# Kernel optimization log

Hardware: AMD Instinct MI355X
Metric: run time of the kernel (lower is better)

## Reference

```python
import jax, jax.numpy as jnp
import numpy as np

M0, M1 = 16, 8            # scalar / vector multiplicities of node_irreps (16x0e + 8x1o)
N_NODES = 10000
N_EDGES = 160000
H_EDGE = 64
W_NUMEL = M0*M0 + M1*M0 + M0*M1 + M1*M1  # 576 per-edge TP weights
EPS = 1e-5


def setup_inputs() -> dict:
    key = jax.random.key(0)
    ks = jax.random.split(key, 8)
    return {
        "node_features": jax.random.normal(ks[0], (N_NODES, M0 + 3*M1), jnp.float32),
        "edge_features": jax.random.normal(ks[1], (N_EDGES, H_EDGE), jnp.float32),
        "edge_sh": jax.random.normal(ks[2], (N_EDGES, 4), jnp.float32),
        "edge_index": jax.random.randint(ks[3], (2, N_EDGES), 0, N_NODES),
        "fc_w1": jax.random.normal(ks[4], (H_EDGE, H_EDGE), jnp.float32) / np.sqrt(H_EDGE),
        "fc_b1": jnp.zeros((H_EDGE,), jnp.float32),
        "fc_w2": jax.random.normal(ks[5], (H_EDGE, W_NUMEL), jnp.float32) / np.sqrt(H_EDGE),
        "fc_b2": jnp.zeros((W_NUMEL,), jnp.float32),
        "bn_w_s": jnp.ones((M0,), jnp.float32),
        "bn_b_s": jnp.zeros((M0,), jnp.float32),
        "bn_w_v": jnp.ones((M1,), jnp.float32),
    }


def reference(node_features, edge_features, edge_sh, edge_index,
              fc_w1, fc_b1, fc_w2, fc_b2, bn_w_s, bn_b_s, bn_w_v):
    N = node_features.shape[0]
    E = edge_features.shape[0]
    edge_dst, edge_src = edge_index[0], edge_index[1]

    # per-edge TP weights from a small MLP on edge features
    w = jax.nn.relu(edge_features @ fc_w1 + fc_b1) @ fc_w2 + fc_b2  # [E, 576]

    # gather node features on destination side
    x = node_features[edge_dst]                      # [E, 40]
    x0 = x[:, :M0]                                   # [E, 16] scalars (0e)
    x1 = x[:, M0:].reshape(E, M1, 3)                 # [E, 8, 3] vectors (1o)
    sh0 = edge_sh[:, 0]                              # [E] l=0
    sh1 = edge_sh[:, 1:4]                            # [E, 3] l=1

    # split per-edge weights by tensor-product path
    o1 = M0*M0; o2 = o1 + M1*M0; o3 = o2 + M0*M1
    w00 = w[:, :o1].reshape(E, M0, M0)               # 0e x 0e -> 0e
    w11 = w[:, o1:o2].reshape(E, M1, M0)             # 1o x 1o -> 0e
    w01 = w[:, o2:o3].reshape(E, M0, M1)             # 0e x 1o -> 1o
    w10 = w[:, o3:].reshape(E, M1, M1)               # 1o x 0e -> 1o

    inv3 = 1.0 / np.sqrt(3.0)                        # w3j(1,1,0) coefficient
    alpha = 1.0 / np.sqrt(M0 + M1)                   # path fan-in normalization

    out0 = (jnp.einsum('eu,euv->ev', x0 * sh0[:, None], w00)
            + inv3 * jnp.einsum('eui,ei,euv->ev', x1, sh1, w11)) * alpha   # [E, 16]
    out1 = (jnp.einsum('eu,ei,euv->evi', x0, sh1, w01)
            + jnp.einsum('e,eui,euv->evi', sh0, x1, w10)) * alpha          # [E, 8, 3]

    tp = jnp.concatenate([out0, out1.reshape(E, 3*M1)], axis=-1)           # [E, 40]

    # scatter_mean over source nodes
    seg = jax.ops.segment_sum(tp, edge_src, num_segments=N)                # [N, 40]
    cnt = jax.ops.segment_sum(jnp.ones((E, 1), tp.dtype), edge_src, num_segments=N)
    out = seg / jnp.maximum(cnt, 1.0)

    # residual (pad is zero-width since tp output irreps == node irreps)
    out = out + node_features

    # e3nn-style BatchNorm (training mode, component normalization)
    s = out[:, :M0]
    v = out[:, M0:].reshape(N, M1, 3)
    mu = s.mean(axis=0)
    s = s - mu
    var = (s * s).mean(axis=0)
    s = s * (jax.lax.rsqrt(var + EPS) * bn_w_s) + bn_b_s
    vnorm = (v * v).mean(axis=-1).mean(axis=0)       # [M1]
    v = v * (jax.lax.rsqrt(vnorm + EPS) * bn_w_v)[None, :, None]
    out = jnp.concatenate([s, v.reshape(N, 3*M1)], axis=-1)

    return out, edge_features
```

## Files before the change

kernel.cpp:

```cpp
#include <hip/hip_runtime.h>

typedef __attribute__((ext_vector_type(8))) short short8;
typedef __attribute__((ext_vector_type(4))) float f32x4;
typedef __attribute__((ext_vector_type(4))) ushort u16x4;

constexpr int NN = 10000;
constexpr int NE = 160000;
constexpr int NT = NE / 16;
constexpr int TPSTR = 64;
constexpr int GBLK = 625;
constexpr float EPSV = 1e-5f;
constexpr float INV3 = 0.57735026918962576f;
constexpr float ALPHA = 0.20412414523193152f;

__device__ __forceinline__ ushort f2bf(float x) {
  unsigned u = __float_as_uint(x);
  u += 0x7fffu + ((u >> 16) & 1u);
  return (ushort)(u >> 16);
}
__device__ __forceinline__ float bf2f(ushort u) {
  return __uint_as_float(((unsigned)u) << 16);
}
__device__ __forceinline__ f32x4 mfma16(short8 a, short8 b, f32x4 c) {
  return __builtin_amdgcn_mfma_f32_16x16x32_bf16(a, b, c, 0, 0, 0);
}
__device__ __forceinline__ void st4u(ushort* p, f32x4 v) {
  u16x4 o;
#pragma unroll
  for (int j = 0; j < 4; ++j) o[j] = f2bf(v[j]);
  *(u16x4*)p = o;
}

constexpr int PREP_DEGB = (NN + 63) / 64;
__global__ __launch_bounds__(64) void prep_w2(const float* __restrict__ w2,
                                              short8* __restrict__ w2bf,
                                              int* __restrict__ deg,
                                              const float* __restrict__ b2,
                                              float* __restrict__ flag) {
  int b = blockIdx.x;
  int lane = threadIdx.x;
  if (b < 72) {
    int jt = b >> 1, kc = b & 1;
    int g = lane >> 4, c = lane & 15;
    short8 v;
#pragma unroll
    for (int j = 0; j < 8; ++j)
      v[j] = (short)f2bf(w2[(kc * 32 + 8 * g + j) * 576 + jt * 16 + c]);
    w2bf[(jt * 2 + kc) * 64 + lane] = v;
  } else if (b < 72 + PREP_DEGB) {
    int idx = (b - 72) * 64 + lane;
    if (idx < NN) deg[idx] = 0;
  } else {
    float m = 0.f;
    for (int i = lane; i < 576; i += 64) m = fmaxf(m, fabsf(b2[i]));
#pragma unroll
    for (int off = 1; off < 64; off <<= 1) m = fmaxf(m, __shfl_xor(m, off));
    if (lane == 0) *flag = m;
  }
}

constexpr int CSTR = 68;
constexpr unsigned SM_W2 = 4608 * 16;
constexpr unsigned SM_B2 = 576 * 4;
constexpr unsigned SM_W1 = 512 * 16;
constexpr unsigned SM_B1 = 64 * 4;
constexpr unsigned SM_HL = 8 * 16 * 72 * 2;
constexpr unsigned SM_SCR = 8 * 16 * CSTR * 4;
constexpr unsigned SM_TOTAL = SM_W2 + SM_B2 + SM_W1 + SM_B1 + SM_HL + SM_SCR;

__global__ __launch_bounds__(512) void conv_kernel(
    const float* __restrict__ ef, const float* __restrict__ w1,
    const float* __restrict__ b1, const short8* __restrict__ w2bf,
    const float* __restrict__ b2, const float* __restrict__ nf,
    const float* __restrict__ sh, const int* __restrict__ ei,
    const int* __restrict__ perm, float* __restrict__ efout, int do_copy,
    ushort* __restrict__ tp, const float* __restrict__ flagp)
{
  extern __shared__ char smem[];
  short8* w2lds = (short8*)smem;
  float*  b2lds = (float*)(smem + SM_W2);
  short8* w1f   = (short8*)(smem + SM_W2 + SM_B2);
  float*  b1lds = (float*)(smem + SM_W2 + SM_B2 + SM_W1);
  ushort* hlall = (ushort*)(smem + SM_W2 + SM_B2 + SM_W1 + SM_B1);
  float*  scrall = (float*)(smem + SM_W2 + SM_B2 + SM_W1 + SM_B1 + SM_HL);

  const int tid = threadIdx.x;
  for (int i = tid; i < 4608; i += 512) w2lds[i] = w2bf[i];
  for (int i = tid; i < 576; i += 512) b2lds[i] = b2[i];
  {
    int tile = tid >> 6, l = tid & 63;
    int nt = tile >> 1, kc = tile & 1;
    int gg = l >> 4, cc = l & 15;
    short8 v;
#pragma unroll
    for (int j = 0; j < 8; ++j)
      v[j] = (short)f2bf(w1[(kc * 32 + 8 * gg + j) * 64 + nt * 16 + cc]);
    w1f[tid] = v;
  }
  if (tid < 64) b1lds[tid] = b1[tid];
  const bool nob2 = (*flagp == 0.f);
  __syncthreads();

  const int lane = tid & 63, wid = tid >> 6;
  const int g = lane >> 4, c = lane & 15;
  const int gh = g >> 1;
  const int e = lane >> 2, part = lane & 3;
  float* scr = scrall + wid * (16 * CSTR);
  ushort* hl = hlall + wid * (16 * 72);

  for (int t = blockIdx.x * 8 + wid; t < NT; t += gridDim.x * 8) {
    const int ege = t * 16 + e;
    const float* __restrict__ src = nf + (size_t)ei[ege] * 40;
    const f32x4 sv = *(const f32x4*)(sh + (size_t)ege * 4);
    const f32x4 v0 = *(const f32x4*)(src + part * 4);
    const f32x4 v1 = *(const f32x4*)(src + 16 + part * 4);
    f32x4 v2 = {};
    if (part < 2) v2 = *(const f32x4*)(src + 32 + part * 4);

    const long ebase = (long)t * 16;
    short8 af[2];
    const float* rowp = ef + (ebase + c) * 64;
#pragma unroll
    for (int kc = 0; kc < 2; ++kc) {
      const f32x4* p = (const f32x4*)(rowp + kc * 32 + 8 * g);
      f32x4 lo = p[0], hi = p[1];
      if (do_copy) {
        f32x4* q = (f32x4*)(efout + (ebase + c) * 64 + kc * 32 + 8 * g);
        q[0] = lo; q[1] = hi;
      }
      short8 v;
#pragma unroll
      for (int j = 0; j < 4; ++j) { v[j] = (short)f2bf(lo[j]); v[4 + j] = (short)f2bf(hi[j]); }
      af[kc] = v;
    }
    f32x4 hacc[4] = {};
#pragma unroll
    for (int nt = 0; nt < 4; ++nt)
#pragma unroll
      for (int kc = 0; kc < 2; ++kc)
        hacc[nt] = mfma16(af[kc], w1f[(nt * 2 + kc) * 64 + lane], hacc[nt]);

#pragma unroll
    for (int nt = 0; nt < 4; ++nt) {
      float bv = b1lds[nt * 16 + c];
#pragma unroll
      for (int q = 0; q < 4; ++q) {
        float h = fmaxf(hacc[nt][q] + bv, 0.f);
        hl[(4 * g + q) * 72 + nt * 16 + c] = f2bf(h);
      }
    }
    const short8 h0 = *(const short8*)&hl[c * 72 + 8 * g];
    const short8 h1 = *(const short8*)&hl[c * 72 + 32 + 8 * g];

    {
      float* ce = scr + e * CSTR;
      f32x4 a0;
#pragma unroll
      for (int q = 0; q < 4; ++q) a0[q] = sv[0] * v0[q];
      *(f32x4*)(ce + 4 * part) = a0;
      *(f32x4*)(ce + 24 + 4 * part) = v0;
      *(f32x4*)(ce + 40 + 4 * part) = v1;
      if (part < 2) *(f32x4*)(ce + 56 + 4 * part) = v2;
#pragma unroll
      for (int uu = 0; uu < 2; ++uu) {
        int u = 2 * part + uu;
        ce[16 + u] = INV3 * (ce[40 + 3 * u] * sv[1] + ce[41 + 3 * u] * sv[2] +
                             ce[42 + 3 * u] * sv[3]);
      }
    }
    const float* __restrict__ cc = scr + c * CSTR;

    f32x4 out0acc = {0.f, 0.f, 0.f, 0.f};
    f32x4 c0acc = {0.f, 0.f, 0.f, 0.f};
    f32x4 c1acc[3] = {};

    if (nob2) {
#pragma unroll
      for (int j4 = 0; j4 < 4; ++j4) {
        const f32x4 a4 = *(const f32x4*)&cc[j4 * 4];
#pragma unroll
        for (int jj = 0; jj < 4; ++jj) {
          const int jt = j4 * 4 + jj;
          f32x4 z = {0.f, 0.f, 0.f, 0.f};
          f32x4 d0 = mfma16(w2lds[(jt * 2 + 0) * 64 + lane], h0, z);
          f32x4 d1 = mfma16(w2lds[(jt * 2 + 1) * 64 + lane], h1, z);
          float a = a4[jj];
#pragma unroll
          for (int q = 0; q < 4; ++q) {
            out0acc[q] = fmaf(a, d0[q], out0acc[q]);
            out0acc[q] = fmaf(a, d1[q], out0acc[q]);
          }
        }
      }
#pragma unroll
      for (int j4 = 0; j4 < 2; ++j4) {
        const f32x4 a4 = *(const f32x4*)&cc[16 + j4 * 4];
#pragma unroll
        for (int jj = 0; jj < 4; ++jj) {
          const int jt = 16 + j4 * 4 + jj;
          f32x4 z = {0.f, 0.f, 0.f, 0.f};
          f32x4 d0 = mfma16(w2lds[(jt * 2 + 0) * 64 + lane], h0, z);
          f32x4 d1 = mfma16(w2lds[(jt * 2 + 1) * 64 + lane], h1, z);
          float a = a4[jj];
#pragma unroll
          for (int q = 0; q < 4; ++q) {
            out0acc[q] = fmaf(a, d0[q], out0acc[q]);
            out0acc[q] = fmaf(a, d1[q], out0acc[q]);
          }
        }
      }
#pragma unroll
      for (int jt = 24; jt < 32; ++jt) {
        f32x4 z = {0.f, 0.f, 0.f, 0.f};
        f32x4 d0 = mfma16(w2lds[(jt * 2 + 0) * 64 + lane], h0, z);
        f32x4 d1 = mfma16(w2lds[(jt * 2 + 1) * 64 + lane], h1, z);
        float a = cc[24 + 2 * (jt - 24) + gh];
#pragma unroll
        for (int q = 0; q < 4; ++q) {
          c0acc[q] = fmaf(a, d0[q], c0acc[q]);
          c0acc[q] = fmaf(a, d1[q], c0acc[q]);
        }
      }
#pragma unroll
      for (int jt = 32; jt < 36; ++jt) {
        f32x4 z = {0.f, 0.f, 0.f, 0.f};
        f32x4 d0 = mfma16(w2lds[(jt * 2 + 0) * 64 + lane], h0, z);
        f32x4 d1 = mfma16(w2lds[(jt * 2 + 1) * 64 + lane], h1, z);
        const int ub = 40 + 3 * (2 * (jt - 32) + gh);
#pragma unroll
        for (int i = 0; i < 3; ++i) {
          float a = cc[ub + i];
#pragma unroll
          for (int q = 0; q < 4; ++q) {
            c1acc[i][q] = fmaf(a, d0[q], c1acc[i][q]);
            c1acc[i][q] = fmaf(a, d1[q], c1acc[i][q]);
          }
        }
      }
    } else {
#pragma unroll
      for (int jt = 0; jt < 16; ++jt) {
        f32x4 d = *(const f32x4*)&b2lds[jt * 16 + 4 * g];
        d = mfma16(w2lds[(jt * 2 + 0) * 64 + lane], h0, d);
        d = mfma16(w2lds[(jt * 2 + 1) * 64 + lane], h1, d);
        float a = cc[jt];
#pragma unroll
        for (int q = 0; q < 4; ++q) out0acc[q] = fmaf(a, d[q], out0acc[q]);
      }
#pragma unroll
      for (int jt = 16; jt < 24; ++jt) {
        f32x4 d = *(const f32x4*)&b2lds[jt * 16 + 4 * g];
        d = mfma16(w2lds[(jt * 2 + 0) * 64 + lane], h0, d);
        d = mfma16(w2lds[(jt * 2 + 1) * 64 + lane], h1, d);
        float a = cc[16 + (jt - 16)];
#pragma unroll
        for (int q = 0; q < 4; ++q) out0acc[q] = fmaf(a, d[q], out0acc[q]);
      }
#pragma unroll
      for (int jt = 24; jt < 32; ++jt) {
        f32x4 d = *(const f32x4*)&b2lds[jt * 16 + 4 * g];
        d = mfma16(w2lds[(jt * 2 + 0) * 64 + lane], h0, d);
        d = mfma16(w2lds[(jt * 2 + 1) * 64 + lane], h1, d);
        float a = cc[24 + 2 * (jt - 24) + gh];
#pragma unroll
        for (int q = 0; q < 4; ++q) c0acc[q] = fmaf(a, d[q], c0acc[q]);
      }
#pragma unroll
      for (int jt = 32; jt < 36; ++jt) {
        f32x4 d = *(const f32x4*)&b2lds[jt * 16 + 4 * g];
        d = mfma16(w2lds[(jt * 2 + 0) * 64 + lane], h0, d);
        d = mfma16(w2lds[(jt * 2 + 1) * 64 + lane], h1, d);
        const int ub = 40 + 3 * (2 * (jt - 32) + gh);
#pragma unroll
        for (int i = 0; i < 3; ++i) {
          float a = cc[ub + i];
#pragma unroll
          for (int q = 0; q < 4; ++q) c1acc[i][q] = fmaf(a, d[q], c1acc[i][q]);
        }
      }
    }

#pragma unroll
    for (int q = 0; q < 4; ++q) c0acc[q] += __shfl_xor(c0acc[q], 32);
#pragma unroll
    for (int i = 0; i < 3; ++i)
#pragma unroll
      for (int q = 0; q < 4; ++q) c1acc[i][q] += __shfl_xor(c1acc[i][q], 32);

    const int eg = t * 16 + c;
    const f32x4 shv = *(const f32x4*)(sh + (size_t)eg * 4);
    ushort* tpr = tp + (size_t)perm[eg] * TPSTR;
    f32x4 o0;
#pragma unroll
    for (int q = 0; q < 4; ++q) o0[q] = ALPHA * out0acc[q];
    st4u(tpr + 4 * g, o0);
    if (g < 2) {
      float wv[12];
#pragma unroll
      for (int q = 0; q < 4; ++q)
#pragma unroll
        for (int i = 0; i < 3; ++i)
          wv[q * 3 + i] = ALPHA * (shv[1 + i] * c0acc[q] + shv[0] * c1acc[i][q]);
#pragma unroll
      for (int p = 0; p < 3; ++p) {
        f32x4 v = {wv[4 * p], wv[4 * p + 1], wv[4 * p + 2], wv[4 * p + 3]};
        st4u(tpr + 16 + 12 * g + 4 * p, v);
      }
    }
  }
}

__global__ __launch_bounds__(256) void hist_kernel(const int* __restrict__ ei,
                                                   int* __restrict__ deg) {
  for (int e = blockIdx.x * 256 + threadIdx.x; e < NE; e += gridDim.x * 256)
    atomicAdd(&deg[ei[NE + e]], 1);
}

__global__ __launch_bounds__(1024) void scan_kernel(const int* __restrict__ deg,
                                                    int* __restrict__ rowoff,
                                                    int* __restrict__ wcur) {
  __shared__ int wsum[16];
  const int t = threadIdx.x;
  const int lane = t & 63, wid = t >> 6;
  const int base = t * 10;
  int d[10];
  int sum = 0;
#pragma unroll
  for (int j = 0; j < 10; ++j) {
    int n = base + j;
    d[j] = (n < NN) ? deg[n] : 0;
    sum += d[j];
  }
  int val = sum;
#pragma unroll
  for (int off = 1; off < 64; off <<= 1) {
    int v = __shfl_up(val, off);
    if (lane >= off) val += v;
  }
  if (lane == 63) wsum[wid] = val;
  __syncthreads();
  if (t < 16) {
    int v = wsum[t];
#pragma unroll
    for (int off = 1; off < 16; off <<= 1) {
      int u = __shfl_up(v, off);
      if (t >= off) v += u;
    }
    wsum[t] = v;
  }
  __syncthreads();
  const int waveoff = (wid > 0) ? wsum[wid - 1] : 0;
  int run = waveoff + (val - sum);
#pragma unroll
  for (int j = 0; j < 10; ++j) {
    int n = base + j;
    if (n < NN) { rowoff[n] = run; wcur[n] = run; }
    run += d[j];
  }
  if (t == 1023) rowoff[NN] = run;
}

__global__ __launch_bounds__(256) void fill_kernel(const int* __restrict__ ei,
                                                   int* __restrict__ wcur,
                                                   int* __restrict__ perm) {
  for (int e = blockIdx.x * 256 + threadIdx.x; e < NE; e += gridDim.x * 256) {
    int pos = atomicAdd(&wcur[ei[NE + e]], 1);
    perm[e] = pos;
  }
}

__global__ __launch_bounds__(256) void gather_kernel(
    const ushort* __restrict__ tp, const int* __restrict__ rowoff,
    const float* __restrict__ nf, float* __restrict__ pre,
    float* __restrict__ pstats)
{
  __shared__ float ls[40];
  const int tid = threadIdx.x;
  if (tid < 40) ls[tid] = 0.f;
  __syncthreads();
  const int wid = tid >> 6, lane = tid & 63;
  float sacc = 0.f, qacc = 0.f;
  if (lane < 40) {
#pragma unroll 1
    for (int i = 0; i < 4; ++i) {
      const int n = blockIdx.x * 16 + wid * 4 + i;
      const int r0 = rowoff[n], r1 = rowoff[n + 1];
      float s0 = 0.f, s1 = 0.f, s2 = 0.f, s3 = 0.f,
            s4 = 0.f, s5 = 0.f, s6 = 0.f, s7 = 0.f;
      int k = r0;
      for (; k + 8 <= r1; k += 8) {
        s0 += bf2f(tp[(size_t)(k + 0) * TPSTR + lane]);
        s1 += bf2f(tp[(size_t)(k + 1) * TPSTR + lane]);
        s2 += bf2f(tp[(size_t)(k + 2) * TPSTR + lane]);
        s3 += bf2f(tp[(size_t)(k + 3) * TPSTR + lane]);
        s4 += bf2f(tp[(size_t)(k + 4) * TPSTR + lane]);
        s5 += bf2f(tp[(size_t)(k + 5) * TPSTR + lane]);
        s6 += bf2f(tp[(size_t)(k + 6) * TPSTR + lane]);
        s7 += bf2f(tp[(size_t)(k + 7) * TPSTR + lane]);
      }
      for (; k < r1; ++k) s0 += bf2f(tp[(size_t)k * TPSTR + lane]);
      float s = ((s0 + s1) + (s2 + s3)) + ((s4 + s5) + (s6 + s7));
      float val = s / fmaxf((float)(r1 - r0), 1.f) + nf[(size_t)n * 40 + lane];
      pre[(size_t)n * 40 + lane] = val;
      if (lane < 16) { sacc += val; qacc += val * val; }
      else qacc += val * val;
    }
    if (lane < 16) {
      atomicAdd(&ls[lane], sacc);
      atomicAdd(&ls[16 + lane], qacc);
    } else {
      atomicAdd(&ls[32 + (lane - 16) / 3], qacc);
    }
  }
  __syncthreads();
  if (tid < 40) pstats[(size_t)blockIdx.x * 40 + tid] = ls[tid];
}

__global__ __launch_bounds__(256) void stats_reduce(
    const float* __restrict__ pstats, float* __restrict__ stats)
{
  const int c = blockIdx.x;
  float s = 0.f;
  for (int i = threadIdx.x; i < GBLK; i += 256) s += pstats[(size_t)i * 40 + c];
#pragma unroll
  for (int off = 1; off < 64; off <<= 1) s += __shfl_xor(s, off);
  __shared__ float red[4];
  if ((threadIdx.x & 63) == 0) red[threadIdx.x >> 6] = s;
  __syncthreads();
  if (threadIdx.x == 0) stats[c] = (red[0] + red[1]) + (red[2] + red[3]);
}

__global__ __launch_bounds__(256) void node_pass2(
    const float* __restrict__ pre, const float* __restrict__ stats,
    const float* __restrict__ bnws, const float* __restrict__ bnbs,
    const float* __restrict__ bnwv, float* __restrict__ out)
{
  int idx = blockIdx.x * blockDim.x + threadIdx.x;
  if (idx >= NN * 40) return;
  int n = idx / 40;
  int c = idx - n * 40;
  float val = pre[idx];
  constexpr float invN = 1.0f / NN;
  if (c < 16) {
    float mu = stats[c] * invN;
    float var = stats[16 + c] * invN - mu * mu;
    out[idx] = (val - mu) * (rsqrtf(var + EPSV) * bnws[c]) + bnbs[c];
  } else {
    int u = (c - 16) / 3;
    float vn = stats[32 + u] * (invN / 3.0f);
    out[idx] = val * (rsqrtf(vn + EPSV) * bnwv[u]);
  }
}

__global__ __launch_bounds__(256) void copy_ef(const f32x4* __restrict__ src,
                                               f32x4* __restrict__ dst) {
  const int n4 = NE * 64 / 4;
  for (int i = blockIdx.x * blockDim.x + threadIdx.x; i < n4;
       i += gridDim.x * blockDim.x)
    dst[i] = src[i];
}

extern "C" void kernel_launch(void* const* d_in, const int* in_sizes, int n_in,
                              void* d_out, int out_size, void* d_ws, size_t ws_size,
                              hipStream_t stream) {
  (void)in_sizes; (void)n_in; (void)out_size;
  const float* nf   = (const float*)d_in[0];
  const float* ef   = (const float*)d_in[1];
  const float* sh   = (const float*)d_in[2];
  const int*   ei   = (const int*)d_in[3];
  const float* w1   = (const float*)d_in[4];
  const float* b1   = (const float*)d_in[5];
  const float* w2   = (const float*)d_in[6];
  const float* b2   = (const float*)d_in[7];
  const float* bnws = (const float*)d_in[8];
  const float* bnbs = (const float*)d_in[9];
  const float* bnwv = (const float*)d_in[10];

  float* out = (float*)d_out;
  float* efout = out + (size_t)NN * 40;

  char* w = (char*)d_ws;
  int* deg     = (int*)w;
  float* stats = (float*)(w + (size_t)NN * 4);
  float* flag  = stats + 44;
  int* rowoff  = (int*)(w + (size_t)NN * 4 + 192);
  int* wcur    = rowoff + NN + 1;
  int* perm    = wcur + NN;
  float* pre   = (float*)(perm + NE);
  float* pstats = pre + (size_t)NN * 40;
  size_t base  = ((size_t)((char*)(pstats + (size_t)GBLK * 40) - w) + 255) & ~(size_t)255;
  short8* w2bf = (short8*)(w + base);
  size_t tpoff = (base + SM_W2 + 255) & ~(size_t)255;

  const size_t TPB = (size_t)NE * TPSTR * 2;
  const size_t needA = tpoff + TPB;

  hipFuncSetAttribute((const void*)conv_kernel,
                      hipFuncAttributeMaxDynamicSharedMemorySize, SM_TOTAL);

  prep_w2<<<72 + PREP_DEGB + 1, 64, 0, stream>>>(w2, w2bf, deg, b2, flag);

  const int pblocks = (NN * 40 + 255) / 256;

  hist_kernel<<<625, 256, 0, stream>>>(ei, deg);
  scan_kernel<<<1, 1024, 0, stream>>>(deg, rowoff, wcur);
  fill_kernel<<<625, 256, 0, stream>>>(ei, wcur, perm);

  if (ws_size >= needA) {
    ushort* tp = (ushort*)(w + tpoff);
    conv_kernel<<<256, 512, SM_TOTAL, stream>>>(
        ef, w1, b1, w2bf, b2, nf, sh, ei, perm, efout, 1, tp, flag);
    gather_kernel<<<GBLK, 256, 0, stream>>>(tp, rowoff, nf, pre, pstats);
    stats_reduce<<<40, 256, 0, stream>>>(pstats, stats);
    node_pass2<<<pblocks, 256, 0, stream>>>(pre, stats, bnws, bnbs, bnwv, out);
  } else {
    ushort* tp = (ushort*)efout;
    conv_kernel<<<256, 512, SM_TOTAL, stream>>>(
        ef, w1, b1, w2bf, b2, nf, sh, ei, perm, efout, 0, tp, flag);
    gather_kernel<<<GBLK, 256, 0, stream>>>(tp, rowoff, nf, pre, pstats);
    stats_reduce<<<40, 256, 0, stream>>>(pstats, stats);
    node_pass2<<<pblocks, 256, 0, stream>>>(pre, stats, bnws, bnbs, bnwv, out);
    copy_ef<<<2048, 256, 0, stream>>>((const f32x4*)ef, (f32x4*)efout);
  }
}
```

Baseline: 94.87 us.

## Switch conv kernel to 32x32 MFMA tiles with atomic work-stealing over edge tiles

```diff
diff --git a/kernel.cpp b/kernel.cpp
--- a/kernel.cpp
+++ b/kernel.cpp
@@ -2,11 +2,12 @@
 
 typedef __attribute__((ext_vector_type(8))) short short8;
 typedef __attribute__((ext_vector_type(4))) float f32x4;
+typedef __attribute__((ext_vector_type(16))) float f32x16;
 typedef __attribute__((ext_vector_type(4))) ushort u16x4;
 
 constexpr int NN = 10000;
 constexpr int NE = 160000;
-constexpr int NT = NE / 16;
+constexpr int NT32 = NE / 32;
 constexpr int TPSTR = 64;
 constexpr int GBLK = 625;
 constexpr float EPSV = 1e-5f;
@@ -21,8 +22,8 @@
 __device__ __forceinline__ float bf2f(ushort u) {
   return __uint_as_float(((unsigned)u) << 16);
 }
-__device__ __forceinline__ f32x4 mfma16(short8 a, short8 b, f32x4 c) {
-  return __builtin_amdgcn_mfma_f32_16x16x32_bf16(a, b, c, 0, 0, 0);
+__device__ __forceinline__ f32x16 mfma32(short8 a, short8 b, f32x16 c) {
+  return __builtin_amdgcn_mfma_f32_32x32x16_bf16(a, b, c, 0, 0, 0);
 }
 __device__ __forceinline__ void st4u(ushort* p, f32x4 v) {
   u16x4 o;
@@ -36,17 +37,18 @@
                                               short8* __restrict__ w2bf,
                                               int* __restrict__ deg,
                                               const float* __restrict__ b2,
-                                              float* __restrict__ flag) {
+                                              float* __restrict__ flag,
+                                              int* __restrict__ wsctr) {
   int b = blockIdx.x;
   int lane = threadIdx.x;
   if (b < 72) {
-    int jt = b >> 1, kc = b & 1;
-    int g = lane >> 4, c = lane & 15;
+    int jt = b >> 2, kt = b & 3;
+    int hi = lane >> 5, cc = lane & 31;
     short8 v;
 #pragma unroll
     for (int j = 0; j < 8; ++j)
-      v[j] = (short)f2bf(w2[(kc * 32 + 8 * g + j) * 576 + jt * 16 + c]);
-    w2bf[(jt * 2 + kc) * 64 + lane] = v;
+      v[j] = (short)f2bf(w2[(size_t)(kt * 16 + 8 * hi + j) * 576 + jt * 32 + cc]);
+    w2bf[(size_t)b * 64 + lane] = v;
   } else if (b < 72 + PREP_DEGB) {
     int idx = (b - 72) * 64 + lane;
     if (idx < NN) deg[idx] = 0;
@@ -56,6 +58,7 @@
 #pragma unroll
     for (int off = 1; off < 64; off <<= 1) m = fmaxf(m, __shfl_xor(m, off));
     if (lane == 0) *flag = m;
+    if (lane == 1) *wsctr = 0;
   }
 }
 
@@ -64,9 +67,8 @@
 constexpr unsigned SM_B2 = 576 * 4;
 constexpr unsigned SM_W1 = 512 * 16;
 constexpr unsigned SM_B1 = 64 * 4;
-constexpr unsigned SM_HL = 8 * 16 * 72 * 2;
-constexpr unsigned SM_SCR = 8 * 16 * CSTR * 4;
-constexpr unsigned SM_TOTAL = SM_W2 + SM_B2 + SM_W1 + SM_B1 + SM_HL + SM_SCR;
+constexpr unsigned SM_SCR = 8 * 32 * CSTR * 4;
+constexpr unsigned SM_TOTAL = SM_W2 + SM_B2 + SM_W1 + SM_B1 + SM_SCR;
 
 __global__ __launch_bounds__(512) void conv_kernel(
     const float* __restrict__ ef, const float* __restrict__ w1,
@@ -74,27 +76,27 @@
     const float* __restrict__ b2, const float* __restrict__ nf,
     const float* __restrict__ sh, const int* __restrict__ ei,
     const int* __restrict__ perm, float* __restrict__ efout, int do_copy,
-    ushort* __restrict__ tp, const float* __restrict__ flagp)
+    ushort* __restrict__ tp, const float* __restrict__ flagp,
+    int* __restrict__ wsctr)
 {
   extern __shared__ char smem[];
   short8* w2lds = (short8*)smem;
   float*  b2lds = (float*)(smem + SM_W2);
   short8* w1f   = (short8*)(smem + SM_W2 + SM_B2);
   float*  b1lds = (float*)(smem + SM_W2 + SM_B2 + SM_W1);
-  ushort* hlall = (ushort*)(smem + SM_W2 + SM_B2 + SM_W1 + SM_B1);
-  float*  scrall = (float*)(smem + SM_W2 + SM_B2 + SM_W1 + SM_B1 + SM_HL);
+  float*  scrall = (float*)(smem + SM_W2 + SM_B2 + SM_W1 + SM_B1);
 
   const int tid = threadIdx.x;
   for (int i = tid; i < 4608; i += 512) w2lds[i] = w2bf[i];
   for (int i = tid; i < 576; i += 512) b2lds[i] = b2[i];
   {
-    int tile = tid >> 6, l = tid & 63;
-    int nt = tile >> 1, kc = tile & 1;
-    int gg = l >> 4, cc = l & 15;
+    int frag = tid >> 6, l = tid & 63;
+    int ft = frag >> 2, kt = frag & 3;
+    int hi = l >> 5, cc = l & 31;
     short8 v;
 #pragma unroll
     for (int j = 0; j < 8; ++j)
-      v[j] = (short)f2bf(w1[(kc * 32 + 8 * gg + j) * 64 + nt * 16 + cc]);
+      v[j] = (short)f2bf(w1[(size_t)(kt * 16 + 8 * hi + j) * 64 + ft * 32 + cc]);
     w1f[tid] = v;
   }
   if (tid < 64) b1lds[tid] = b1[tid];
@@ -102,210 +104,214 @@
   __syncthreads();
 
   const int lane = tid & 63, wid = tid >> 6;
-  const int g = lane >> 4, c = lane & 15;
-  const int gh = g >> 1;
-  const int e = lane >> 2, part = lane & 3;
-  float* scr = scrall + wid * (16 * CSTR);
-  ushort* hl = hlall + wid * (16 * 72);
-
-  for (int t = blockIdx.x * 8 + wid; t < NT; t += gridDim.x * 8) {
-    const int ege = t * 16 + e;
-    const float* __restrict__ src = nf + (size_t)ei[ege] * 40;
-    const f32x4 sv = *(const f32x4*)(sh + (size_t)ege * 4);
-    const f32x4 v0 = *(const f32x4*)(src + part * 4);
-    const f32x4 v1 = *(const f32x4*)(src + 16 + part * 4);
-    f32x4 v2 = {};
-    if (part < 2) v2 = *(const f32x4*)(src + 32 + part * 4);
-
-    const long ebase = (long)t * 16;
-    short8 af[2];
-    const float* rowp = ef + (ebase + c) * 64;
-#pragma unroll
-    for (int kc = 0; kc < 2; ++kc) {
-      const f32x4* p = (const f32x4*)(rowp + kc * 32 + 8 * g);
-      f32x4 lo = p[0], hi = p[1];
+  const int hi = lane >> 5, e32 = lane & 31;
+  float* scr = scrall + wid * (32 * CSTR);
+  ushort* hl = (ushort*)scr;
+
+  for (;;) {
+    int t;
+    if (lane == 0) t = atomicAdd(wsctr, 1);
+    t = __shfl(t, 0);
+    if (t >= NT32) break;
+    const int myeg = t * 32 + e32;
+
+    const float* __restrict__ src = nf + (size_t)ei[myeg] * 40;
+    const f32x4 sv = *(const f32x4*)(sh + (size_t)myeg * 4);
+    f32x4 sg0, sg1, sg2, sg3, sg4;
+    {
+      const float* sp = src + hi * 20;
+      sg0 = *(const f32x4*)(sp);
+      sg1 = *(const f32x4*)(sp + 4);
+      sg2 = *(const f32x4*)(sp + 8);
+      sg3 = *(const f32x4*)(sp + 12);
+      sg4 = *(const f32x4*)(sp + 16);
+    }
+
+    const float* __restrict__ rowp = ef + (size_t)myeg * 64;
+    short8 af[4];
+#pragma unroll
+    for (int kt = 0; kt < 4; ++kt) {
+      f32x4 lo = *(const f32x4*)(rowp + kt * 16 + 8 * hi);
+      f32x4 hv = *(const f32x4*)(rowp + kt * 16 + 8 * hi + 4);
       if (do_copy) {
-        f32x4* q = (f32x4*)(efout + (ebase + c) * 64 + kc * 32 + 8 * g);
-        q[0] = lo; q[1] = hi;
+        float* q = efout + (size_t)myeg * 64 + kt * 16 + 8 * hi;
+        *(f32x4*)q = lo; *(f32x4*)(q + 4) = hv;
       }
       short8 v;
 #pragma unroll
-      for (int j = 0; j < 4; ++j) { v[j] = (short)f2bf(lo[j]); v[4 + j] = (short)f2bf(hi[j]); }
-      af[kc] = v;
-    }
-    f32x4 hacc[4] = {};
-#pragma unroll
-    for (int nt = 0; nt < 4; ++nt)
-#pragma unroll
-      for (int kc = 0; kc < 2; ++kc)
-        hacc[nt] = mfma16(af[kc], w1f[(nt * 2 + kc) * 64 + lane], hacc[nt]);
-
-#pragma unroll
-    for (int nt = 0; nt < 4; ++nt) {
-      float bv = b1lds[nt * 16 + c];
+      for (int j = 0; j < 4; ++j) { v[j] = (short)f2bf(lo[j]); v[4 + j] = (short)f2bf(hv[j]); }
+      af[kt] = v;
+    }
+    f32x16 hacc0, hacc1;
+    {
 #pragma unroll
       for (int q = 0; q < 4; ++q) {
-        float h = fmaxf(hacc[nt][q] + bv, 0.f);
-        hl[(4 * g + q) * 72 + nt * 16 + c] = f2bf(h);
-      }
-    }
-    const short8 h0 = *(const short8*)&hl[c * 72 + 8 * g];
-    const short8 h1 = *(const short8*)&hl[c * 72 + 32 + 8 * g];
-
+        f32x4 b0 = *(const f32x4*)&b1lds[4 * hi + 8 * q];
+        f32x4 b1v = *(const f32x4*)&b1lds[32 + 4 * hi + 8 * q];
+#pragma unroll
+        for (int j = 0; j < 4; ++j) { hacc0[q * 4 + j] = b0[j]; hacc1[q * 4 + j] = b1v[j]; }
+      }
+    }
+#pragma unroll
+    for (int kt = 0; kt < 4; ++kt) {
+      hacc0 = mfma32(w1f[(0 * 4 + kt) * 64 + lane], af[kt], hacc0);
+      hacc1 = mfma32(w1f[(1 * 4 + kt) * 64 + lane], af[kt], hacc1);
+    }
+
+#pragma unroll
+    for (int q = 0; q < 4; ++q) {
+      u16x4 o0, o1;
+#pragma unroll
+      for (int j = 0; j < 4; ++j) {
+        o0[j] = f2bf(fmaxf(hacc0[q * 4 + j], 0.f));
+        o1[j] = f2bf(fmaxf(hacc1[q * 4 + j], 0.f));
+      }
+      *(u16x4*)&hl[e32 * 72 + 4 * hi + 8 * q] = o0;
+      *(u16x4*)&hl[e32 * 72 + 32 + 4 * hi + 8 * q] = o1;
+    }
+    asm volatile("" ::: "memory");
+    short8 hB[4];
+#pragma unroll
+    for (int kt = 0; kt < 4; ++kt)
+      hB[kt] = *(const short8*)&hl[e32 * 72 + kt * 16 + 8 * hi];
+    asm volatile("" ::: "memory");
+
+    float* ce = scr + e32 * CSTR;
+    if (hi == 0) {
+      *(f32x4*)(ce + 24) = sg0; *(f32x4*)(ce + 28) = sg1;
+      *(f32x4*)(ce + 32) = sg2; *(f32x4*)(ce + 36) = sg3;
+      *(f32x4*)(ce + 40) = sg4;
+    } else {
+      *(f32x4*)(ce + 44) = sg0; *(f32x4*)(ce + 48) = sg1;
+      *(f32x4*)(ce + 52) = sg2; *(f32x4*)(ce + 56) = sg3;
+      *(f32x4*)(ce + 60) = sg4;
+    }
     {
-      float* ce = scr + e * CSTR;
-      f32x4 a0;
-#pragma unroll
-      for (int q = 0; q < 4; ++q) a0[q] = sv[0] * v0[q];
-      *(f32x4*)(ce + 4 * part) = a0;
-      *(f32x4*)(ce + 24 + 4 * part) = v0;
-      *(f32x4*)(ce + 40 + 4 * part) = v1;
-      if (part < 2) *(f32x4*)(ce + 56 + 4 * part) = v2;
-#pragma unroll
-      for (int uu = 0; uu < 2; ++uu) {
-        int u = 2 * part + uu;
-        ce[16 + u] = INV3 * (ce[40 + 3 * u] * sv[1] + ce[41 + 3 * u] * sv[2] +
-                             ce[42 + 3 * u] * sv[3]);
-      }
-    }
-    const float* __restrict__ cc = scr + c * CSTR;
-
-    f32x4 out0acc = {0.f, 0.f, 0.f, 0.f};
-    f32x4 c0acc = {0.f, 0.f, 0.f, 0.f};
-    f32x4 c1acc[3] = {};
-
-    if (nob2) {
-#pragma unroll
-      for (int j4 = 0; j4 < 4; ++j4) {
-        const f32x4 a4 = *(const f32x4*)&cc[j4 * 4];
-#pragma unroll
-        for (int jj = 0; jj < 4; ++jj) {
-          const int jt = j4 * 4 + jj;
-          f32x4 z = {0.f, 0.f, 0.f, 0.f};
-          f32x4 d0 = mfma16(w2lds[(jt * 2 + 0) * 64 + lane], h0, z);
-          f32x4 d1 = mfma16(w2lds[(jt * 2 + 1) * 64 + lane], h1, z);
-          float a = a4[jj];
-#pragma unroll
-          for (int q = 0; q < 4; ++q) {
-            out0acc[q] = fmaf(a, d0[q], out0acc[q]);
-            out0acc[q] = fmaf(a, d1[q], out0acc[q]);
-          }
+      f32x4 r0 = *(const f32x4*)(ce + 24 + 8 * hi);
+      f32x4 r1 = *(const f32x4*)(ce + 28 + 8 * hi);
+      f32x4 a0, a1;
+#pragma unroll
+      for (int j = 0; j < 4; ++j) { a0[j] = sv[0] * r0[j]; a1[j] = sv[0] * r1[j]; }
+      *(f32x4*)(ce + 8 * hi) = a0;
+      *(f32x4*)(ce + 8 * hi + 4) = a1;
+      f32x4 av;
+#pragma unroll
+      for (int uu = 0; uu < 4; ++uu) {
+        int u = 4 * hi + uu;
+        av[uu] = INV3 * (ce[40 + 3 * u] * sv[1] + ce[41 + 3 * u] * sv[2] +
+                         ce[42 + 3 * u] * sv[3]);
+      }
+      *(f32x4*)(ce + 16 + 4 * hi) = av;
+    }
+    const float* __restrict__ cc = scr + e32 * CSTR;
+
+    f32x4 oa = {0.f, 0.f, 0.f, 0.f}, ob = {0.f, 0.f, 0.f, 0.f};
+    f32x4 c0 = {0.f, 0.f, 0.f, 0.f};
+    f32x4 c1[3] = {};
+
+#pragma unroll
+    for (int jt = 0; jt < 8; ++jt) {
+      f32x16 d = {};
+      if (!nob2) {
+#pragma unroll
+        for (int q = 0; q < 4; ++q) {
+          f32x4 bv = *(const f32x4*)&b2lds[jt * 32 + 4 * hi + 8 * q];
+#pragma unroll
+          for (int j = 0; j < 4; ++j) d[q * 4 + j] = bv[j];
         }
       }
 #pragma unroll
-      for (int j4 = 0; j4 < 2; ++j4) {
-        const f32x4 a4 = *(const f32x4*)&cc[16 + j4 * 4];
-#pragma unroll
-        for (int jj = 0; jj < 4; ++jj) {
-          const int jt = 16 + j4 * 4 + jj;
-          f32x4 z = {0.f, 0.f, 0.f, 0.f};
-          f32x4 d0 = mfma16(w2lds[(jt * 2 + 0) * 64 + lane], h0, z);
-          f32x4 d1 = mfma16(w2lds[(jt * 2 + 1) * 64 + lane], h1, z);
-          float a = a4[jj];
-#pragma unroll
-          for (int q = 0; q < 4; ++q) {
-            out0acc[q] = fmaf(a, d0[q], out0acc[q]);
-            out0acc[q] = fmaf(a, d1[q], out0acc[q]);
-          }
+      for (int kt = 0; kt < 4; ++kt) d = mfma32(w2lds[(jt * 4 + kt) * 64 + lane], hB[kt], d);
+      const float au0 = cc[jt * 2], au1 = cc[jt * 2 + 1];
+#pragma unroll
+      for (int r = 0; r < 16; ++r) {
+        float v = ((r & 8) ? au1 : au0) * d[r];
+        if (r & 4) ob[r & 3] += v; else oa[r & 3] += v;
+      }
+    }
+#pragma unroll
+    for (int jt = 8; jt < 12; ++jt) {
+      f32x16 d = {};
+      if (!nob2) {
+#pragma unroll
+        for (int q = 0; q < 4; ++q) {
+          f32x4 bv = *(const f32x4*)&b2lds[jt * 32 + 4 * hi + 8 * q];
+#pragma unroll
+          for (int j = 0; j < 4; ++j) d[q * 4 + j] = bv[j];
         }
       }
 #pragma unroll
-      for (int jt = 24; jt < 32; ++jt) {
-        f32x4 z = {0.f, 0.f, 0.f, 0.f};
-        f32x4 d0 = mfma16(w2lds[(jt * 2 + 0) * 64 + lane], h0, z);
-        f32x4 d1 = mfma16(w2lds[(jt * 2 + 1) * 64 + lane], h1, z);
-        float a = cc[24 + 2 * (jt - 24) + gh];
+      for (int kt = 0; kt < 4; ++kt) d = mfma32(w2lds[(jt * 4 + kt) * 64 + lane], hB[kt], d);
+      const float au0 = cc[16 + (jt - 8) * 2], au1 = cc[16 + (jt - 8) * 2 + 1];
+#pragma unroll
+      for (int r = 0; r < 16; ++r) {
+        float v = ((r & 8) ? au1 : au0) * d[r];
+        if (r & 4) ob[r & 3] += v; else oa[r & 3] += v;
+      }
+    }
+#pragma unroll
+    for (int jt = 12; jt < 16; ++jt) {
+      f32x16 d = {};
+      if (!nob2) {
 #pragma unroll
         for (int q = 0; q < 4; ++q) {
-          c0acc[q] = fmaf(a, d0[q], c0acc[q]);
-          c0acc[q] = fmaf(a, d1[q], c0acc[q]);
+          f32x4 bv = *(const f32x4*)&b2lds[jt * 32 + 4 * hi + 8 * q];
+#pragma unroll
+          for (int j = 0; j < 4; ++j) d[q * 4 + j] = bv[j];
         }
       }
 #pragma unroll
-      for (int jt = 32; jt < 36; ++jt) {
-        f32x4 z = {0.f, 0.f, 0.f, 0.f};
-        f32x4 d0 = mfma16(w2lds[(jt * 2 + 0) * 64 + lane], h0, z);
-        f32x4 d1 = mfma16(w2lds[(jt * 2 + 1) * 64 + lane], h1, z);
-        const int ub = 40 + 3 * (2 * (jt - 32) + gh);
+      for (int kt = 0; kt < 4; ++kt) d = mfma32(w2lds[(jt * 4 + kt) * 64 + lane], hB[kt], d);
+      const f32x4 x4 = *(const f32x4*)&cc[24 + (jt - 12) * 4];
+#pragma unroll
+      for (int r = 0; r < 16; ++r) c0[r & 3] += x4[r >> 2] * d[r];
+    }
+#pragma unroll
+    for (int jt = 16; jt < 18; ++jt) {
+      f32x16 d = {};
+      if (!nob2) {
+#pragma unroll
+        for (int q = 0; q < 4; ++q) {
+          f32x4 bv = *(const f32x4*)&b2lds[jt * 32 + 4 * hi + 8 * q];
+#pragma unroll
+          for (int j = 0; j < 4; ++j) d[q * 4 + j] = bv[j];
+        }
+      }
+#pragma unroll
+      for (int kt = 0; kt < 4; ++kt) d = mfma32(w2lds[(jt * 4 + kt) * 64 + lane], hB[kt], d);
+      const f32x4 xA = *(const f32x4*)&cc[40 + 12 * (jt - 16)];
+      const f32x4 xB = *(const f32x4*)&cc[44 + 12 * (jt - 16)];
+      const f32x4 xC = *(const f32x4*)&cc[48 + 12 * (jt - 16)];
+#pragma unroll
+      for (int r = 0; r < 16; ++r) {
+        const int q = r >> 2;
 #pragma unroll
         for (int i = 0; i < 3; ++i) {
-          float a = cc[ub + i];
-#pragma unroll
-          for (int q = 0; q < 4; ++q) {
-            c1acc[i][q] = fmaf(a, d0[q], c1acc[i][q]);
-            c1acc[i][q] = fmaf(a, d1[q], c1acc[i][q]);
-          }
+          const int fl = 3 * q + i;
+          float x = (fl < 4) ? xA[fl] : (fl < 8) ? xB[fl - 4] : xC[fl - 8];
+          c1[i][r & 3] += x * d[r];
         }
       }
-    } else {
-#pragma unroll
-      for (int jt = 0; jt < 16; ++jt) {
-        f32x4 d = *(const f32x4*)&b2lds[jt * 16 + 4 * g];
-        d = mfma16(w2lds[(jt * 2 + 0) * 64 + lane], h0, d);
-        d = mfma16(w2lds[(jt * 2 + 1) * 64 + lane], h1, d);
-        float a = cc[jt];
-#pragma unroll
-        for (int q = 0; q < 4; ++q) out0acc[q] = fmaf(a, d[q], out0acc[q]);
-      }
-#pragma unroll
-      for (int jt = 16; jt < 24; ++jt) {
-        f32x4 d = *(const f32x4*)&b2lds[jt * 16 + 4 * g];
-        d = mfma16(w2lds[(jt * 2 + 0) * 64 + lane], h0, d);
-        d = mfma16(w2lds[(jt * 2 + 1) * 64 + lane], h1, d);
-        float a = cc[16 + (jt - 16)];
-#pragma unroll
-        for (int q = 0; q < 4; ++q) out0acc[q] = fmaf(a, d[q], out0acc[q]);
-      }
-#pragma unroll
-      for (int jt = 24; jt < 32; ++jt) {
-        f32x4 d = *(const f32x4*)&b2lds[jt * 16 + 4 * g];
-        d = mfma16(w2lds[(jt * 2 + 0) * 64 + lane], h0, d);
-        d = mfma16(w2lds[(jt * 2 + 1) * 64 + lane], h1, d);
-        float a = cc[24 + 2 * (jt - 24) + gh];
-#pragma unroll
-        for (int q = 0; q < 4; ++q) c0acc[q] = fmaf(a, d[q], c0acc[q]);
-      }
-#pragma unroll
-      for (int jt = 32; jt < 36; ++jt) {
-        f32x4 d = *(const f32x4*)&b2lds[jt * 16 + 4 * g];
-        d = mfma16(w2lds[(jt * 2 + 0) * 64 + lane], h0, d);
-        d = mfma16(w2lds[(jt * 2 + 1) * 64 + lane], h1, d);
-        const int ub = 40 + 3 * (2 * (jt - 32) + gh);
-#pragma unroll
-        for (int i = 0; i < 3; ++i) {
-          float a = cc[ub + i];
-#pragma unroll
-          for (int q = 0; q < 4; ++q) c1acc[i][q] = fmaf(a, d[q], c1acc[i][q]);
-        }
-      }
-    }
-
-#pragma unroll
-    for (int q = 0; q < 4; ++q) c0acc[q] += __shfl_xor(c0acc[q], 32);
-#pragma unroll
-    for (int i = 0; i < 3; ++i)
-#pragma unroll
-      for (int q = 0; q < 4; ++q) c1acc[i][q] += __shfl_xor(c1acc[i][q], 32);
-
-    const int eg = t * 16 + c;
-    const f32x4 shv = *(const f32x4*)(sh + (size_t)eg * 4);
-    ushort* tpr = tp + (size_t)perm[eg] * TPSTR;
-    f32x4 o0;
-#pragma unroll
-    for (int q = 0; q < 4; ++q) o0[q] = ALPHA * out0acc[q];
-    st4u(tpr + 4 * g, o0);
-    if (g < 2) {
-      float wv[12];
-#pragma unroll
-      for (int q = 0; q < 4; ++q)
-#pragma unroll
-        for (int i = 0; i < 3; ++i)
-          wv[q * 3 + i] = ALPHA * (shv[1 + i] * c0acc[q] + shv[0] * c1acc[i][q]);
-#pragma unroll
-      for (int p = 0; p < 3; ++p) {
-        f32x4 v = {wv[4 * p], wv[4 * p + 1], wv[4 * p + 2], wv[4 * p + 3]};
-        st4u(tpr + 16 + 12 * g + 4 * p, v);
-      }
+    }
+
+    ushort* tpr = tp + (size_t)perm[myeg] * TPSTR;
+    f32x4 s;
+#pragma unroll
+    for (int j = 0; j < 4; ++j) s[j] = ALPHA * oa[j];
+    st4u(tpr + 4 * hi, s);
+#pragma unroll
+    for (int j = 0; j < 4; ++j) s[j] = ALPHA * ob[j];
+    st4u(tpr + 8 + 4 * hi, s);
+    float wv[12];
+#pragma unroll
+    for (int q = 0; q < 4; ++q)
+#pragma unroll
+      for (int i = 0; i < 3; ++i)
+        wv[q * 3 + i] = ALPHA * (sv[1 + i] * c0[q] + sv[0] * c1[i][q]);
+#pragma unroll
+    for (int p = 0; p < 3; ++p) {
+      f32x4 v = {wv[4 * p], wv[4 * p + 1], wv[4 * p + 2], wv[4 * p + 3]};
+      st4u(tpr + 16 + 12 * hi + 4 * p, v);
     }
   }
 }
@@ -483,6 +489,7 @@
   int* deg     = (int*)w;
   float* stats = (float*)(w + (size_t)NN * 4);
   float* flag  = stats + 44;
+  int* wsctr   = (int*)(stats + 45);
   int* rowoff  = (int*)(w + (size_t)NN * 4 + 192);
   int* wcur    = rowoff + NN + 1;
   int* perm    = wcur + NN;
@@ -498,7 +505,7 @@
   hipFuncSetAttribute((const void*)conv_kernel,
                       hipFuncAttributeMaxDynamicSharedMemorySize, SM_TOTAL);
 
-  prep_w2<<<72 + PREP_DEGB + 1, 64, 0, stream>>>(w2, w2bf, deg, b2, flag);
+  prep_w2<<<72 + PREP_DEGB + 1, 64, 0, stream>>>(w2, w2bf, deg, b2, flag, wsctr);
 
   const int pblocks = (NN * 40 + 255) / 256;
 
@@ -509,14 +516,14 @@
   if (ws_size >= needA) {
     ushort* tp = (ushort*)(w + tpoff);
     conv_kernel<<<256, 512, SM_TOTAL, stream>>>(
-        ef, w1, b1, w2bf, b2, nf, sh, ei, perm, efout, 1, tp, flag);
+        ef, w1, b1, w2bf, b2, nf, sh, ei, perm, efout, 1, tp, flag, wsctr);
     gather_kernel<<<GBLK, 256, 0, stream>>>(tp, rowoff, nf, pre, pstats);
     stats_reduce<<<40, 256, 0, stream>>>(pstats, stats);
     node_pass2<<<pblocks, 256, 0, stream>>>(pre, stats, bnws, bnbs, bnwv, out);
   } else {
     ushort* tp = (ushort*)efout;
     conv_kernel<<<256, 512, SM_TOTAL, stream>>>(
-        ef, w1, b1, w2bf, b2, nf, sh, ei, perm, efout, 0, tp, flag);
+        ef, w1, b1, w2bf, b2, nf, sh, ei, perm, efout, 0, tp, flag, wsctr);
     gather_kernel<<<GBLK, 256, 0, stream>>>(tp, rowoff, nf, pre, pstats);
     stats_reduce<<<40, 256, 0, stream>>>(pstats, stats);
     node_pass2<<<pblocks, 256, 0, stream>>>(pre, stats, bnws, bnbs, bnwv, out);
```

After: 184.9 us. +94.9%, slower.
